# Kernel optimization log

Measured on AMD Instinct MI355X. Metric: run time of the kernel, lower is better.

Reference implementation:

```python
import jax, jax.numpy as jnp
import numpy as np

DIM = 64
HEAD_DIM = 4
NUM_HEADS = DIM // HEAD_DIM  # 16
ATTN_DIM = NUM_HEADS * HEAD_DIM  # 64
BN_EPS = 1e-5


def setup_inputs() -> dict:
    key = jax.random.key(0)
    k_x, k_qkv, k_proj, k_g, k_b, k_m, k_v = jax.random.split(key, 7)
    B, C, H, W = 8, DIM, 64, 64
    x = jax.random.normal(k_x, (B, C, H, W), dtype=jnp.float32)
    # nn.Linear(dim, 3*attn_dim, bias=False): y = x @ W^T; store transposed for x @ w
    w_qkv = jax.random.normal(k_qkv, (DIM, 3 * ATTN_DIM), dtype=jnp.float32) * (DIM ** -0.5)
    w_proj = jax.random.normal(k_proj, (ATTN_DIM, DIM), dtype=jnp.float32) * (ATTN_DIM ** -0.5)
    gamma = 1.0 + 0.1 * jax.random.normal(k_g, (DIM,), dtype=jnp.float32)
    beta = 0.1 * jax.random.normal(k_b, (DIM,), dtype=jnp.float32)
    bn_mean = 0.1 * jax.random.normal(k_m, (DIM,), dtype=jnp.float32)
    bn_var = jnp.abs(jax.random.normal(k_v, (DIM,), dtype=jnp.float32)) + 0.5
    return {"x": x, "w_qkv": w_qkv, "w_proj": w_proj, "gamma": gamma,
            "beta": beta, "bn_mean": bn_mean, "bn_var": bn_var}


def _forward(x, w_qkv, w_proj, gamma, beta, bn_mean, bn_var):
    B, C, H, W = x.shape
    Hp, Wp = H // 2, W // 2
    N = Hp * Wp
    # ---- MaxPool2d(2,2) with indices (non-overlapping windows) ----
    xr = x.reshape(B, C, Hp, 2, Wp, 2).transpose(0, 1, 2, 4, 3, 5).reshape(B, C, Hp, Wp, 4)
    idx = jnp.argmax(xr, axis=-1)              # [B,C,Hp,Wp] window-local argmax
    pooled = jnp.max(xr, axis=-1)              # [B,C,Hp,Wp]
    # ---- GA attention on pooled map ----
    t = pooled.transpose(0, 2, 3, 1).reshape(B, N, C)          # [B,N,C]
    qkv = (t @ w_qkv).reshape(B, N, 3, NUM_HEADS, HEAD_DIM)
    q, k, v = qkv[:, :, 0], qkv[:, :, 1], qkv[:, :, 2]          # [B,N,h,d]
    scale = HEAD_DIM ** -0.5
    attn = jnp.einsum('bnhd,bmhd->bhnm', q, k) * scale          # [B,h,N,N]
    attn = jax.nn.softmax(attn, axis=-1)
    o = jnp.einsum('bhnm,bmhd->bnhd', attn, v).reshape(B, N, ATTN_DIM)
    o = (o @ w_proj).reshape(B, Hp, Wp, C).transpose(0, 3, 1, 2)  # [B,C,Hp,Wp]
    # ---- BatchNorm2d (eval mode, running stats) ----
    inv = gamma / jnp.sqrt(bn_var + BN_EPS)
    o = o * inv[:, None, None] + (beta - bn_mean * inv)[:, None, None]
    # ---- MaxUnpool2d(2,2): scatter to argmax positions ----
    oh = jax.nn.one_hot(idx, 4, dtype=o.dtype)                  # [B,C,Hp,Wp,4]
    up = oh * o[..., None]
    out = up.reshape(B, C, Hp, Wp, 2, 2).transpose(0, 1, 2, 4, 3, 5).reshape(B, C, H, W)
    return out


def reference(x, w_qkv, w_proj, gamma, beta, bn_mean, bn_var):
    return _forward(x, w_qkv, w_proj, gamma, beta, bn_mean, bn_var)
```

## Files before the change

kernel.cpp:

```cpp
#include <hip/hip_runtime.h>
#include <hip/hip_bf16.h>


typedef float    f32x4 __attribute__((ext_vector_type(4)));
typedef _Float16 f16x8 __attribute__((ext_vector_type(8)));
typedef unsigned int uint32_tt;

__global__ __launch_bounds__(256) void pool_kernel(const float* __restrict__ x,
                                                   float* __restrict__ t,
                                                   int* __restrict__ idx) {
    int g = blockIdx.x * 256 + threadIdx.x;
    int wp = g & 31, hp = (g >> 5) & 31, c = (g >> 10) & 63, b = g >> 16;
    const float* px = x + (((b * 64 + c) * 64 + 2 * hp) * 64 + 2 * wp);
    float2 r0 = *(const float2*)px;
    float2 r1 = *(const float2*)(px + 64);
    float best = r0.x; int bi = 0;
    if (r0.y > best) { best = r0.y; bi = 1; }
    if (r1.x > best) { best = r1.x; bi = 2; }
    if (r1.y > best) { best = r1.y; bi = 3; }
    int n = hp * 32 + wp;
    t[(b * 1024 + n) * 64 + c] = best;
    idx[g] = bi;
}

__global__ __launch_bounds__(192) void qkv_kernel(const float* __restrict__ t,
                                                  const float* __restrict__ w_qkv,
                                                  float* __restrict__ q,
                                                  float* __restrict__ k,
                                                  float* __restrict__ v) {
    __shared__ float trow[16 * 64];
    int tid = threadIdx.x;
    int row0 = blockIdx.x * 16;
    for (int i = tid; i < 1024; i += 192) trow[i] = t[row0 * 64 + i];
    int j  = tid % 96;
    int rh = tid / 96;
    float wc0[64], wc1[64];
    #pragma unroll
    for (int c = 0; c < 64; c++) {
        wc0[c] = w_qkv[c * 192 + j];
        wc1[c] = w_qkv[c * 192 + j + 96];
    }
    __syncthreads();
    int s0 = j >> 6, h0 = (j >> 2) & 15, d0 = j & 3;
    int j1 = j + 96;
    int s1 = j1 >> 6, h1 = (j1 >> 2) & 15, d1 = j1 & 3;
    float* dst0 = (s0 == 0) ? q : (s0 == 1) ? k : v;
    float* dst1 = (s1 == 0) ? q : (s1 == 1) ? k : v;
    for (int r = 0; r < 8; r++) {
        int row = rh * 8 + r;
        const float4* tr = (const float4*)&trow[row * 64];
        float a0 = 0.f, a1 = 0.f;
        #pragma unroll
        for (int c4 = 0; c4 < 16; c4++) {
            float4 tv = tr[c4];
            a0 += tv.x * wc0[c4 * 4] + tv.y * wc0[c4 * 4 + 1]
                + tv.z * wc0[c4 * 4 + 2] + tv.w * wc0[c4 * 4 + 3];
            a1 += tv.x * wc1[c4 * 4] + tv.y * wc1[c4 * 4 + 1]
                + tv.z * wc1[c4 * 4 + 2] + tv.w * wc1[c4 * 4 + 3];
        }
        int ng = row0 + row, b = ng >> 10, n = ng & 1023;
        dst0[((b * 16 + h0) * 1024 + n) * 4 + d0] = a0;
        dst1[((b * 16 + h1) * 1024 + n) * 4 + d1] = a1;
    }
}

__global__ __launch_bounds__(256) void attn_kernel(const float* __restrict__ q,
                                                   const float* __restrict__ k,
                                                   const float* __restrict__ v,
                                                   float* __restrict__ o) {
    __shared__ __align__(16) unsigned char smem[27840];
    f16x8*          Kh2 = (f16x8*)smem;
    unsigned short* VTu = (unsigned short*)(smem + 16384);
    float*          lsc = (float*)(smem + 26784);
    int bh = blockIdx.x >> 3;
    int row0 = (blockIdx.x & 7) * 128;
    int tid = threadIdx.x;
    const float4* kp4 = (const float4*)(k + bh * 4096);
    const float4* vp4 = (const float4*)(v + bh * 4096);
    #pragma unroll
    for (int i = 0; i < 4; i++) {
        int key = i * 256 + tid;
        float4 kf = kp4[key];
        f16x8 kk;
        kk[0] = (_Float16)kf.x; kk[4] = (_Float16)(kf.x - (float)kk[0]);
        kk[1] = (_Float16)kf.y; kk[5] = (_Float16)(kf.y - (float)kk[1]);
        kk[2] = (_Float16)kf.z; kk[6] = (_Float16)(kf.z - (float)kk[2]);
        kk[3] = (_Float16)kf.w; kk[7] = (_Float16)(kf.w - (float)kk[3]);
        Kh2[key] = kk;
        float4 vf = vp4[key];
        int pos = (key & ~31) | (((key & 15) >> 2) << 3)
                | (((key >> 4) & 1) << 2) | (key & 3);
        VTu[0 * 1040 + pos] = __builtin_bit_cast(unsigned short, (_Float16)vf.x);
        VTu[1 * 1040 + pos] = __builtin_bit_cast(unsigned short, (_Float16)vf.y);
        VTu[2 * 1040 + pos] = __builtin_bit_cast(unsigned short, (_Float16)vf.z);
        VTu[3 * 1040 + pos] = __builtin_bit_cast(unsigned short, (_Float16)vf.w);
        VTu[4 * 1040 + key] = 0x3C00;
    }
    int w = tid >> 6, lane = tid & 63;
    int c = lane & 15, quad = lane >> 4;
    int mv = (c < 5) ? c : 4;
    const float C1 = 0.5f * 1.44269504088896f;
    const float4* qp4 = (const float4*)(q + bh * 4096);
    f16x8 bq[2];
    #pragma unroll
    for (int s = 0; s < 2; s++) {
        int rowg = row0 + w * 32 + s * 16 + c;
        float4 qv = qp4[rowg];
        float qx = qv.x * C1, qy = qv.y * C1, qz = qv.z * C1, qw = qv.w * C1;
        _Float16 hx = (_Float16)qx, hy = (_Float16)qy,
                 hz = (_Float16)qz, hw = (_Float16)qw;
        _Float16 gx = (_Float16)(qx - (float)hx), gy = (_Float16)(qy - (float)hy),
                 gz = (_Float16)(qz - (float)hz), gw = (_Float16)(qw - (float)hw);
        f16x8 a = {};
        if (quad == 0) {
            a[0] = hx; a[1] = hy; a[2] = hz; a[3] = hw;
            a[4] = hx; a[5] = hy; a[6] = hz; a[7] = hw;
        } else if (quad == 1) {
            a[0] = gx; a[1] = gy; a[2] = gz; a[3] = gw;
            a[4] = gx; a[5] = gy; a[6] = gz; a[7] = gw;
        }
        bq[s] = a;
    }
    __syncthreads();
    f32x4 acc[2];
    acc[0] = (f32x4)(0.f); acc[1] = (f32x4)(0.f);
    const f32x4 cm14 = { -14.f, -14.f, -14.f, -14.f };
    #pragma unroll 2
    for (int T = 0; T < 32; T++) {
        f16x8 ka0 = Kh2[(2 * T) * 16 + c];
        f16x8 ka1 = Kh2[(2 * T + 1) * 16 + c];
        const uint4* vptr = (const uint4*)((const unsigned char*)VTu
                                           + mv * 2080 + T * 64 + quad * 16);
        f16x8 va = __builtin_bit_cast(f16x8, *vptr);
        #pragma unroll
        for (int s = 0; s < 2; s++) {
            f32x4 S0 = __builtin_amdgcn_mfma_f32_16x16x32_f16(ka0, bq[s], cm14, 0, 0, 0);
            f32x4 S1 = __builtin_amdgcn_mfma_f32_16x16x32_f16(ka1, bq[s], cm14, 0, 0, 0);
            float p00 = __builtin_amdgcn_exp2f(S0[0]);
            float p01 = __builtin_amdgcn_exp2f(S0[1]);
            float p02 = __builtin_amdgcn_exp2f(S0[2]);
            float p03 = __builtin_amdgcn_exp2f(S0[3]);
            float p10 = __builtin_amdgcn_exp2f(S1[0]);
            float p11 = __builtin_amdgcn_exp2f(S1[1]);
            float p12 = __builtin_amdgcn_exp2f(S1[2]);
            float p13 = __builtin_amdgcn_exp2f(S1[3]);
            uint4 pbu;
            pbu.x = __builtin_bit_cast(uint32_tt, __builtin_amdgcn_cvt_pkrtz(p00, p01));
            pbu.y = __builtin_bit_cast(uint32_tt, __builtin_amdgcn_cvt_pkrtz(p02, p03));
            pbu.z = __builtin_bit_cast(uint32_tt, __builtin_amdgcn_cvt_pkrtz(p10, p11));
            pbu.w = __builtin_bit_cast(uint32_tt, __builtin_amdgcn_cvt_pkrtz(p12, p13));
            f16x8 pb = __builtin_bit_cast(f16x8, pbu);
            acc[s] = __builtin_amdgcn_mfma_f32_16x16x32_f16(va, pb, acc[s], 0, 0, 0);
        }
    }
    if (quad == 1) {
        #pragma unroll
        for (int s = 0; s < 2; s++) lsc[w * 32 + s * 16 + c] = acc[s][0];
    }
    __syncthreads();
    if (quad == 0) {
        int b0 = bh >> 4, h = bh & 15;
        #pragma unroll
        for (int s = 0; s < 2; s++) {
            float rl = 1.f / lsc[w * 32 + s * 16 + c];
            int rowg = row0 + w * 32 + s * 16 + c;
            float4 res = { acc[s][0] * rl, acc[s][1] * rl,
                           acc[s][2] * rl, acc[s][3] * rl };
            *(float4*)&o[(b0 * 1024 + rowg) * 64 + h * 4] = res;
        }
    }
}

__global__ __launch_bounds__(256) void proj_kernel(const float* __restrict__ o,
                                                   const float* __restrict__ w_proj,
                                                   const float* __restrict__ gamma,
                                                   const float* __restrict__ beta,
                                                   const float* __restrict__ mean,
                                                   const float* __restrict__ var,
                                                   const int* __restrict__ idx,
                                                   float* __restrict__ out) {
    __shared__ float ws[64 * 64];
    int b = blockIdx.x >> 5, hp = blockIdx.x & 31;
    int tid = threadIdx.x;
    for (int i = tid; i < 4096; i += 256) ws[i] = w_proj[i];
    int wp = tid & 31, cg = tid >> 5;
    float oreg[64];
    const float* orow = o + (b * 1024 + hp * 32 + wp) * 64;
    #pragma unroll
    for (int a4 = 0; a4 < 16; a4++) {
        float4 t4 = ((const float4*)orow)[a4];
        oreg[a4 * 4] = t4.x; oreg[a4 * 4 + 1] = t4.y;
        oreg[a4 * 4 + 2] = t4.z; oreg[a4 * 4 + 3] = t4.w;
    }
    __syncthreads();
    #pragma unroll
    for (int g = 0; g < 2; g++) {
        int c0 = cg * 8 + g * 4;
        float4 acc = {0.f, 0.f, 0.f, 0.f};
        #pragma unroll
        for (int a = 0; a < 64; a++) {
            float4 wv = *(const float4*)&ws[a * 64 + c0];
            acc.x += oreg[a] * wv.x; acc.y += oreg[a] * wv.y;
            acc.z += oreg[a] * wv.z; acc.w += oreg[a] * wv.w;
        }
        float accs[4] = { acc.x, acc.y, acc.z, acc.w };
        #pragma unroll
        for (int i = 0; i < 4; i++) {
            int c = c0 + i;
            float inv = gamma[c] * rsqrtf(var[c] + 1e-5f);
            float val = accs[i] * inv + (beta[c] - mean[c] * inv);
            int id = idx[((b * 64 + c) * 32 + hp) * 32 + wp];
            int base = ((b * 64 + c) * 64 + 2 * hp) * 64 + 2 * wp;
            float2 r0 = { id == 0 ? val : 0.f, id == 1 ? val : 0.f };
            float2 r1 = { id == 2 ? val : 0.f, id == 3 ? val : 0.f };
            *(float2*)&out[base] = r0;
            *(float2*)&out[base + 64] = r1;
        }
    }
}

extern "C" void kernel_launch(void* const* d_in, const int* in_sizes, int n_in,
                              void* d_out, int out_size, void* d_ws, size_t ws_size,
                              hipStream_t stream) {
    const float* x      = (const float*)d_in[0];
    const float* w_qkv  = (const float*)d_in[1];
    const float* w_proj = (const float*)d_in[2];
    const float* gamma  = (const float*)d_in[3];
    const float* beta   = (const float*)d_in[4];
    const float* bn_mean= (const float*)d_in[5];
    const float* bn_var = (const float*)d_in[6];
    float* out = (float*)d_out;

    const int SEG = 524288;
    float* ws = (float*)d_ws;
    float* t   = ws;
    int*   idx = (int*)(ws + SEG);
    float* q   = ws + 2 * SEG;
    float* k   = ws + 3 * SEG;
    float* v   = ws + 4 * SEG;
    float* o   = ws + 5 * SEG;

    pool_kernel<<<2048, 256, 0, stream>>>(x, t, idx);
    qkv_kernel<<<512, 192, 0, stream>>>(t, w_qkv, q, k, v);
    attn_kernel<<<1024, 256, 0, stream>>>(q, k, v, o);
    proj_kernel<<<256, 256, 0, stream>>>(o, w_proj, gamma, beta, bn_mean, bn_var, idx, out);
}
```

Before: 119.1 us.

## Precompute fp16 K split and transposed V once per head in separate prep kernel

Moves the fp16 hi/lo split of K and the swizzled fp16 transpose of V out of the attention kernel into a new prep kernel that runs once per (batch, head). Before, each of the 8 row blocks per head redid that conversion. The attention kernel now copies ready-made tiles into shared memory with wide 16-byte loads and fills the ones row directly. It also sets a minimum-occupancy launch bound. The cost is an extra kernel launch and an extra global write and read of the converted K/V, and the attention kernel still reads the unchanged remainder of shared memory for scores.

```diff
diff --git a/kernel.cpp b/kernel.cpp
--- a/kernel.cpp
+++ b/kernel.cpp
@@ -5,6 +5,12 @@
 typedef float    f32x4 __attribute__((ext_vector_type(4)));
 typedef _Float16 f16x8 __attribute__((ext_vector_type(8)));
 typedef unsigned int uint32_tt;
+
+static __device__ __forceinline__ uint32_tt pk2(float a, float b) {
+    uint32_tt lo = (uint32_tt)__builtin_bit_cast(unsigned short, (_Float16)a);
+    uint32_tt hi = (uint32_tt)__builtin_bit_cast(unsigned short, (_Float16)b);
+    return lo | (hi << 16);
+}
 
 __global__ __launch_bounds__(256) void pool_kernel(const float* __restrict__ x,
                                                    float* __restrict__ t,
@@ -64,19 +70,16 @@
     }
 }
 
-__global__ __launch_bounds__(256) void attn_kernel(const float* __restrict__ q,
-                                                   const float* __restrict__ k,
+__global__ __launch_bounds__(256) void prep_kernel(const float* __restrict__ k,
                                                    const float* __restrict__ v,
-                                                   float* __restrict__ o) {
-    __shared__ __align__(16) unsigned char smem[27840];
-    f16x8*          Kh2 = (f16x8*)smem;
-    unsigned short* VTu = (unsigned short*)(smem + 16384);
-    float*          lsc = (float*)(smem + 26784);
-    int bh = blockIdx.x >> 3;
-    int row0 = (blockIdx.x & 7) * 128;
+                                                   uint4* __restrict__ kg,
+                                                   uint32_tt* __restrict__ vg) {
+    int bh = blockIdx.x;
     int tid = threadIdx.x;
     const float4* kp4 = (const float4*)(k + bh * 4096);
     const float4* vp4 = (const float4*)(v + bh * 4096);
+    uint4* kgb = kg + bh * 1024;
+    uint32_tt* vgb = vg + bh * 2080;
     #pragma unroll
     for (int i = 0; i < 4; i++) {
         int key = i * 256 + tid;
@@ -86,15 +89,48 @@
         kk[1] = (_Float16)kf.y; kk[5] = (_Float16)(kf.y - (float)kk[1]);
         kk[2] = (_Float16)kf.z; kk[6] = (_Float16)(kf.z - (float)kk[2]);
         kk[3] = (_Float16)kf.w; kk[7] = (_Float16)(kf.w - (float)kk[3]);
-        Kh2[key] = kk;
-        float4 vf = vp4[key];
+        kgb[key] = __builtin_bit_cast(uint4, kk);
+    }
+    #pragma unroll
+    for (int i = 0; i < 2; i++) {
+        int m = i * 256 + tid;
+        int key = 2 * m;
+        float4 v0 = vp4[key], v1 = vp4[key + 1];
         int pos = (key & ~31) | (((key & 15) >> 2) << 3)
                 | (((key >> 4) & 1) << 2) | (key & 3);
-        VTu[0 * 1040 + pos] = __builtin_bit_cast(unsigned short, (_Float16)vf.x);
-        VTu[1 * 1040 + pos] = __builtin_bit_cast(unsigned short, (_Float16)vf.y);
-        VTu[2 * 1040 + pos] = __builtin_bit_cast(unsigned short, (_Float16)vf.z);
-        VTu[3 * 1040 + pos] = __builtin_bit_cast(unsigned short, (_Float16)vf.w);
-        VTu[4 * 1040 + key] = 0x3C00;
+        int pw = pos >> 1;
+        vgb[0 * 520 + pw] = pk2(v0.x, v1.x);
+        vgb[1 * 520 + pw] = pk2(v0.y, v1.y);
+        vgb[2 * 520 + pw] = pk2(v0.z, v1.z);
+        vgb[3 * 520 + pw] = pk2(v0.w, v1.w);
+    }
+}
+
+__global__ __launch_bounds__(256, 4) void attn_kernel(const float* __restrict__ q,
+                                                      const uint4* __restrict__ kg,
+                                                      const uint32_tt* __restrict__ vg,
+                                                      float* __restrict__ o) {
+    __shared__ __align__(16) unsigned char smem[27840];
+    f16x8* Kh2 = (f16x8*)smem;
+    float* lsc = (float*)(smem + 26752);
+    int bh = blockIdx.x >> 3;
+    int row0 = (blockIdx.x & 7) * 128;
+    int tid = threadIdx.x;
+    uint4* smem4 = (uint4*)smem;
+    const uint4* kgb = kg + bh * 1024;
+    const uint4* vgb = (const uint4*)(vg + bh * 2080);
+    #pragma unroll
+    for (int i = 0; i < 4; i++)
+        smem4[i * 256 + tid] = kgb[i * 256 + tid];
+    #pragma unroll
+    for (int i = 0; i < 3; i++) {
+        int ix = i * 256 + tid;
+        if (ix < 520) smem4[1024 + ix] = vgb[ix];
+    }
+    {
+        uint32_tt* op = (uint32_tt*)(smem + 24704);
+        op[tid] = 0x3C003C00u;
+        op[256 + tid] = 0x3C003C00u;
     }
     int w = tid >> 6, lane = tid & 63;
     int c = lane & 15, quad = lane >> 4;
@@ -129,7 +165,7 @@
     for (int T = 0; T < 32; T++) {
         f16x8 ka0 = Kh2[(2 * T) * 16 + c];
         f16x8 ka1 = Kh2[(2 * T + 1) * 16 + c];
-        const uint4* vptr = (const uint4*)((const unsigned char*)VTu
+        const uint4* vptr = (const uint4*)(smem + 16384
                                            + mv * 2080 + T * 64 + quad * 16);
         f16x8 va = __builtin_bit_cast(f16x8, *vptr);
         #pragma unroll
@@ -239,9 +275,12 @@
     float* k   = ws + 3 * SEG;
     float* v   = ws + 4 * SEG;
     float* o   = ws + 5 * SEG;
+    uint4*     kg = (uint4*)(ws + 6 * SEG);
+    uint32_tt* vg = (uint32_tt*)(ws + 7 * SEG);
 
     pool_kernel<<<2048, 256, 0, stream>>>(x, t, idx);
     qkv_kernel<<<512, 192, 0, stream>>>(t, w_qkv, q, k, v);
-    attn_kernel<<<1024, 256, 0, stream>>>(q, k, v, o);
+    prep_kernel<<<128, 256, 0, stream>>>(k, v, kg, vg);
+    attn_kernel<<<1024, 256, 0, stream>>>(q, kg, vg, o);
     proj_kernel<<<256, 256, 0, stream>>>(o, w_proj, gamma, beta, bn_mean, bn_var, idx, out);
 }
```

After: 118.0 us. About the same (-0.9%).
